# Performance work log

Measured on AMD Instinct MI355X. Metric: run time of the kernel, lower is better.

## Reference

```python
import jax, jax.numpy as jnp
import numpy as np

N_NODES = 100000
N_EDGES = 600000
FEAT_DIM = 128


def setup_inputs() -> dict:
    key = jax.random.key(0)
    k_x, k_e, k_w1, k_b1, k_w2, k_b2 = jax.random.split(key, 6)
    x = jax.random.normal(k_x, (N_NODES, FEAT_DIM), dtype=jnp.float32)
    edge_index = jax.random.randint(k_e, (2, N_EDGES), 0, N_NODES, dtype=jnp.int64)
    # nn.Linear default init: U(-1/sqrt(fan_in), 1/sqrt(fan_in))
    lim1 = 1.0 / np.sqrt(2 * FEAT_DIM)
    lim2 = 1.0 / np.sqrt(FEAT_DIM)
    W1 = jax.random.uniform(k_w1, (2 * FEAT_DIM, FEAT_DIM), minval=-lim1, maxval=lim1, dtype=jnp.float32)
    b1 = jax.random.uniform(k_b1, (FEAT_DIM,), minval=-lim1, maxval=lim1, dtype=jnp.float32)
    W2 = jax.random.uniform(k_w2, (FEAT_DIM, 1), minval=-lim2, maxval=lim2, dtype=jnp.float32)
    b2 = jax.random.uniform(k_b2, (1,), minval=-lim2, maxval=lim2, dtype=jnp.float32)
    return {"x": x, "edge_index": edge_index, "W1": W1, "b1": b1, "W2": W2, "b2": b2}


def reference(x, edge_index, W1, b1, W2, b2):
    row, col = edge_index[0], edge_index[1]
    # gather endpoint features and concat -> [E, 2*feat_dim]
    edge_feat = jnp.concatenate([x[row], x[col]], axis=1)
    h = jax.nn.relu(edge_feat @ W1 + b1)  # [E, feat_dim]
    return jax.nn.sigmoid(h @ W2 + b2)    # [E, 1]
```

## Files before the change

kernel.cpp:

```cpp
#include <hip/hip_runtime.h>
#include <stdint.h>

#define N_NODES 100000
#define N_EDGES 600000
#define FEAT 128
#define BLK_M 128

typedef __attribute__((ext_vector_type(8))) short short8;
typedef __attribute__((ext_vector_type(4))) short sv4;
typedef __attribute__((ext_vector_type(4))) float floatx4;

__device__ __forceinline__ short f2bf(float f) {
    unsigned u = __builtin_bit_cast(unsigned, f);
    u = (u + 0x7FFFu + ((u >> 16) & 1u)) >> 16;
    return (short)u;
}
__device__ __forceinline__ float bf2f(short s) {
    unsigned u = ((unsigned)(unsigned short)s) << 16;
    return __builtin_bit_cast(float, u);
}

__global__ __launch_bounds__(512, 4) void node_gemm_kernel(
    const float* __restrict__ x, const float* __restrict__ w1,
    const float* __restrict__ b1, short* __restrict__ y)
{
    __shared__ short lds_b[16 * 256 * 8];

    const int tid  = threadIdx.x;
    const int lane = tid & 63;
    const int wave = tid >> 6;
    const int nl   = lane & 15;
    const int q    = lane >> 4;
    const int m0   = blockIdx.x * BLK_M + wave * 16;

    const int node = m0 + nl;
    const int nsrc = (node < N_NODES) ? node : 0;
    floatx4 xv[8];
#pragma unroll
    for (int s = 0; s < 4; ++s) {
        const float* p = x + (size_t)nsrc * FEAT + s * 32 + q * 8;
        xv[2 * s]     = *(const floatx4*)(p);
        xv[2 * s + 1] = *(const floatx4*)(p + 4);
    }

#pragma unroll
    for (int it = 0; it < 8; ++it) {
        int t = it * 512 + tid;
        int n = t & 255, c = t >> 8;
        const float* src = (n < 128) ? (w1 + (c * 8) * 128 + n)
                                     : (w1 + (128 + c * 8) * 128 + (n - 128));
        short8 v;
#pragma unroll
        for (int j = 0; j < 8; ++j) v[j] = f2bf(src[j * 128]);
        *(short8*)(lds_b + t * 8) = v;
    }

    __syncthreads();

    short8 a[4];
#pragma unroll
    for (int s = 0; s < 4; ++s) {
        short8 av;
#pragma unroll
        for (int j = 0; j < 8; ++j) av[j] = f2bf(xv[2 * s + (j >> 2)][j & 3]);
        a[s] = av;
    }

    floatx4 acc[16];
#pragma unroll
    for (int nt = 0; nt < 16; ++nt) acc[nt] = (floatx4)(0.0f);

#pragma unroll
    for (int s = 0; s < 4; ++s) {
        const int crow = (s * 4 + q) << 8;
#pragma unroll
        for (int nt = 0; nt < 16; ++nt) {
            short8 wf = *(const short8*)(lds_b + ((crow + nt * 16 + nl) << 3));
            acc[nt] = __builtin_amdgcn_mfma_f32_16x16x32_bf16(wf, a[s], acc[nt], 0, 0, 0);
        }
    }

    if (node < N_NODES) {
        short* yr = y + (size_t)node * 256 + q * 4;
#pragma unroll
        for (int nt = 0; nt < 8; ++nt) {
            floatx4 bb = *(const floatx4*)(b1 + nt * 16 + q * 4);
            sv4 o;
            o[0] = f2bf(acc[nt][0] + bb[0]); o[1] = f2bf(acc[nt][1] + bb[1]);
            o[2] = f2bf(acc[nt][2] + bb[2]); o[3] = f2bf(acc[nt][3] + bb[3]);
            *(sv4*)(yr + nt * 16) = o;
        }
#pragma unroll
        for (int nt = 8; nt < 16; ++nt) {
            sv4 o;
            o[0] = f2bf(acc[nt][0]); o[1] = f2bf(acc[nt][1]);
            o[2] = f2bf(acc[nt][2]); o[3] = f2bf(acc[nt][3]);
            *(sv4*)(yr + nt * 16) = o;
        }
    }
}

__global__ __launch_bounds__(256) void edge_kernel(
    const short* __restrict__ y, const int* __restrict__ eidx,
    const float* __restrict__ w2, const float* __restrict__ b2,
    float* __restrict__ out)
{
    const int l = threadIdx.x & 15;

    float w2r[8];
#pragma unroll
    for (int j = 0; j < 8; ++j) w2r[j] = w2[l * 8 + j];
    const float bias2 = b2[0];

    const int slot   = blockIdx.x * 16 + (threadIdx.x >> 4);
    const int nslots = gridDim.x * 16;

    for (int eb = slot * 4; eb < N_EDGES; eb += nslots * 4) {
        int4 rr = *(const int4*)(eidx + eb);
        int4 cc = *(const int4*)(eidx + N_EDGES + eb);

        short8 u0 = *(const short8*)(y + (size_t)rr.x * 256 + l * 8);
        short8 u1 = *(const short8*)(y + (size_t)rr.y * 256 + l * 8);
        short8 u2 = *(const short8*)(y + (size_t)rr.z * 256 + l * 8);
        short8 u3 = *(const short8*)(y + (size_t)rr.w * 256 + l * 8);
        short8 v0 = *(const short8*)(y + (size_t)cc.x * 256 + 128 + l * 8);
        short8 v1 = *(const short8*)(y + (size_t)cc.y * 256 + 128 + l * 8);
        short8 v2 = *(const short8*)(y + (size_t)cc.z * 256 + 128 + l * 8);
        short8 v3 = *(const short8*)(y + (size_t)cc.w * 256 + 128 + l * 8);

        float p0 = 0.0f, p1 = 0.0f, p2 = 0.0f, p3 = 0.0f;
#pragma unroll
        for (int j = 0; j < 8; ++j) {
            p0 = fmaf(fmaxf(bf2f(u0[j]) + bf2f(v0[j]), 0.0f), w2r[j], p0);
            p1 = fmaf(fmaxf(bf2f(u1[j]) + bf2f(v1[j]), 0.0f), w2r[j], p1);
            p2 = fmaf(fmaxf(bf2f(u2[j]) + bf2f(v2[j]), 0.0f), w2r[j], p2);
            p3 = fmaf(fmaxf(bf2f(u3[j]) + bf2f(v3[j]), 0.0f), w2r[j], p3);
        }
#pragma unroll
        for (int d = 1; d < 16; d <<= 1) {
            p0 += __shfl_xor(p0, d);
            p1 += __shfl_xor(p1, d);
            p2 += __shfl_xor(p2, d);
            p3 += __shfl_xor(p3, d);
        }

        if (l == 0) {
            floatx4 o;
            o[0] = 1.0f / (1.0f + __expf(-(p0 + bias2)));
            o[1] = 1.0f / (1.0f + __expf(-(p1 + bias2)));
            o[2] = 1.0f / (1.0f + __expf(-(p2 + bias2)));
            o[3] = 1.0f / (1.0f + __expf(-(p3 + bias2)));
            *(floatx4*)(out + eb) = o;
        }
    }
}

extern "C" void kernel_launch(void* const* d_in, const int* in_sizes, int n_in,
                              void* d_out, int out_size, void* d_ws, size_t ws_size,
                              hipStream_t stream) {
    const float* x  = (const float*)d_in[0];
    const int*   ei = (const int*)d_in[1];
    const float* W1 = (const float*)d_in[2];
    const float* b1 = (const float*)d_in[3];
    const float* W2 = (const float*)d_in[4];
    const float* b2 = (const float*)d_in[5];
    float* out = (float*)d_out;

    short* ybf = (short*)d_ws;

    int mblocks = (N_NODES + BLK_M - 1) / BLK_M;
    node_gemm_kernel<<<mblocks, 512, 0, stream>>>(x, W1, b1, ybf);

    edge_kernel<<<2048, 256, 0, stream>>>(ybf, ei, W2, b2, out);
}
```

Before: 160.6 us.

## Fuse node GEMM and edge MLP into a single per-edge MFMA kernel

Replaces the two-kernel scheme with one persistent kernel. The old scheme precomputed per-node halves of the first layer into a bf16 table, then gathered and combined them per edge. The new kernel gathers fp32 node features for each edge endpoint, runs the full 256x128 first layer on the matrix cores per 16-edge tile, and applies ReLU, the second layer and the sigmoid in registers. This removes the intermediate table write/read and the second launch. In exchange it recomputes the GEMM for every edge rather than every node, and gathers fp32 rows instead of bf16 halves, which raises both FLOPs and gather traffic.

```diff
diff --git a/kernel.cpp b/kernel.cpp
--- a/kernel.cpp
+++ b/kernel.cpp
@@ -4,10 +4,10 @@
 #define N_NODES 100000
 #define N_EDGES 600000
 #define FEAT 128
-#define BLK_M 128
+#define GRID_F 1024
+#define NWTASK 37500
 
 typedef __attribute__((ext_vector_type(8))) short short8;
-typedef __attribute__((ext_vector_type(4))) short sv4;
 typedef __attribute__((ext_vector_type(4))) float floatx4;
 
 __device__ __forceinline__ short f2bf(float f) {
@@ -15,14 +15,12 @@
     u = (u + 0x7FFFu + ((u >> 16) & 1u)) >> 16;
     return (short)u;
 }
-__device__ __forceinline__ float bf2f(short s) {
-    unsigned u = ((unsigned)(unsigned short)s) << 16;
-    return __builtin_bit_cast(float, u);
-}
 
-__global__ __launch_bounds__(512, 4) void node_gemm_kernel(
-    const float* __restrict__ x, const float* __restrict__ w1,
-    const float* __restrict__ b1, short* __restrict__ y)
+__global__ __launch_bounds__(512, 2) void fused_edge_kernel(
+    const float* __restrict__ x, const int* __restrict__ eidx,
+    const float* __restrict__ w1, const float* __restrict__ b1,
+    const float* __restrict__ w2, const float* __restrict__ b2,
+    float* __restrict__ out)
 {
     __shared__ short lds_b[16 * 256 * 8];
 
@@ -31,17 +29,6 @@
     const int wave = tid >> 6;
     const int nl   = lane & 15;
     const int q    = lane >> 4;
-    const int m0   = blockIdx.x * BLK_M + wave * 16;
-
-    const int node = m0 + nl;
-    const int nsrc = (node < N_NODES) ? node : 0;
-    floatx4 xv[8];
-#pragma unroll
-    for (int s = 0; s < 4; ++s) {
-        const float* p = x + (size_t)nsrc * FEAT + s * 32 + q * 8;
-        xv[2 * s]     = *(const floatx4*)(p);
-        xv[2 * s + 1] = *(const floatx4*)(p + 4);
-    }
 
 #pragma unroll
     for (int it = 0; it < 8; ++it) {
@@ -55,102 +42,91 @@
         *(short8*)(lds_b + t * 8) = v;
     }
 
+    float w2v[8], b1v[8];
+#pragma unroll
+    for (int nt = 0; nt < 8; ++nt) {
+        w2v[nt] = w2[nt * 16 + nl];
+        b1v[nt] = b1[nt * 16 + nl];
+    }
+    const float bias2 = b2[0];
+
     __syncthreads();
 
-    short8 a[4];
+    const int w0     = blockIdx.x * 8 + wave;
+    const int wstep  = GRID_F * 8;
+
+    for (int t = w0; t < NWTASK; t += wstep) {
+        const int e0 = t * 16;
+        const int r = eidx[e0 + nl];
+        const int c = eidx[N_EDGES + e0 + nl];
+        const float* pr = x + (size_t)r * FEAT;
+        const float* pc = x + (size_t)c * FEAT;
+
+        floatx4 xr[8], xc[8];
 #pragma unroll
-    for (int s = 0; s < 4; ++s) {
-        short8 av;
+        for (int s = 0; s < 4; ++s) {
+            xr[2 * s]     = *(const floatx4*)(pr + s * 32 + q * 8);
+            xr[2 * s + 1] = *(const floatx4*)(pr + s * 32 + q * 8 + 4);
+            xc[2 * s]     = *(const floatx4*)(pc + s * 32 + q * 8);
+            xc[2 * s + 1] = *(const floatx4*)(pc + s * 32 + q * 8 + 4);
+        }
+        short8 a1[4], a2[4];
 #pragma unroll
-        for (int j = 0; j < 8; ++j) av[j] = f2bf(xv[2 * s + (j >> 2)][j & 3]);
-        a[s] = av;
-    }
+        for (int s = 0; s < 4; ++s) {
+            short8 v1, v2;
+#pragma unroll
+            for (int j = 0; j < 8; ++j) {
+                v1[j] = f2bf(xr[2 * s + (j >> 2)][j & 3]);
+                v2[j] = f2bf(xc[2 * s + (j >> 2)][j & 3]);
+            }
+            a1[s] = v1; a2[s] = v2;
+        }
 
-    floatx4 acc[16];
+        floatx4 acc[8];
 #pragma unroll
-    for (int nt = 0; nt < 16; ++nt) acc[nt] = (floatx4)(0.0f);
+        for (int nt = 0; nt < 8; ++nt) acc[nt] = (floatx4)(0.0f);
 
 #pragma unroll
-    for (int s = 0; s < 4; ++s) {
-        const int crow = (s * 4 + q) << 8;
+        for (int s = 0; s < 4; ++s) {
+            const int crow = (s * 4 + q) << 8;
 #pragma unroll
-        for (int nt = 0; nt < 16; ++nt) {
-            short8 wf = *(const short8*)(lds_b + ((crow + nt * 16 + nl) << 3));
-            acc[nt] = __builtin_amdgcn_mfma_f32_16x16x32_bf16(wf, a[s], acc[nt], 0, 0, 0);
+            for (int nt = 0; nt < 8; ++nt) {
+                short8 bf = *(const short8*)(lds_b + ((crow + nt * 16 + nl) << 3));
+                acc[nt] = __builtin_amdgcn_mfma_f32_16x16x32_bf16(a1[s], bf, acc[nt], 0, 0, 0);
+            }
         }
-    }
+#pragma unroll
+        for (int s = 0; s < 4; ++s) {
+            const int crow = (s * 4 + q) << 8;
+#pragma unroll
+            for (int nt = 0; nt < 8; ++nt) {
+                short8 bf = *(const short8*)(lds_b + ((crow + 128 + nt * 16 + nl) << 3));
+                acc[nt] = __builtin_amdgcn_mfma_f32_16x16x32_bf16(a2[s], bf, acc[nt], 0, 0, 0);
+            }
+        }
 
-    if (node < N_NODES) {
-        short* yr = y + (size_t)node * 256 + q * 4;
+        float p[4] = {0.0f, 0.0f, 0.0f, 0.0f};
 #pragma unroll
         for (int nt = 0; nt < 8; ++nt) {
-            floatx4 bb = *(const floatx4*)(b1 + nt * 16 + q * 4);
-            sv4 o;
-            o[0] = f2bf(acc[nt][0] + bb[0]); o[1] = f2bf(acc[nt][1] + bb[1]);
-            o[2] = f2bf(acc[nt][2] + bb[2]); o[3] = f2bf(acc[nt][3] + bb[3]);
-            *(sv4*)(yr + nt * 16) = o;
-        }
 #pragma unroll
-        for (int nt = 8; nt < 16; ++nt) {
-            sv4 o;
-            o[0] = f2bf(acc[nt][0]); o[1] = f2bf(acc[nt][1]);
-            o[2] = f2bf(acc[nt][2]); o[3] = f2bf(acc[nt][3]);
-            *(sv4*)(yr + nt * 16) = o;
-        }
-    }
-}
-
-__global__ __launch_bounds__(256) void edge_kernel(
-    const short* __restrict__ y, const int* __restrict__ eidx,
-    const float* __restrict__ w2, const float* __restrict__ b2,
-    float* __restrict__ out)
-{
-    const int l = threadIdx.x & 15;
-
-    float w2r[8];
-#pragma unroll
-    for (int j = 0; j < 8; ++j) w2r[j] = w2[l * 8 + j];
-    const float bias2 = b2[0];
-
-    const int slot   = blockIdx.x * 16 + (threadIdx.x >> 4);
-    const int nslots = gridDim.x * 16;
-
-    for (int eb = slot * 4; eb < N_EDGES; eb += nslots * 4) {
-        int4 rr = *(const int4*)(eidx + eb);
-        int4 cc = *(const int4*)(eidx + N_EDGES + eb);
-
-        short8 u0 = *(const short8*)(y + (size_t)rr.x * 256 + l * 8);
-        short8 u1 = *(const short8*)(y + (size_t)rr.y * 256 + l * 8);
-        short8 u2 = *(const short8*)(y + (size_t)rr.z * 256 + l * 8);
-        short8 u3 = *(const short8*)(y + (size_t)rr.w * 256 + l * 8);
-        short8 v0 = *(const short8*)(y + (size_t)cc.x * 256 + 128 + l * 8);
-        short8 v1 = *(const short8*)(y + (size_t)cc.y * 256 + 128 + l * 8);
-        short8 v2 = *(const short8*)(y + (size_t)cc.z * 256 + 128 + l * 8);
-        short8 v3 = *(const short8*)(y + (size_t)cc.w * 256 + 128 + l * 8);
-
-        float p0 = 0.0f, p1 = 0.0f, p2 = 0.0f, p3 = 0.0f;
-#pragma unroll
-        for (int j = 0; j < 8; ++j) {
-            p0 = fmaf(fmaxf(bf2f(u0[j]) + bf2f(v0[j]), 0.0f), w2r[j], p0);
-            p1 = fmaf(fmaxf(bf2f(u1[j]) + bf2f(v1[j]), 0.0f), w2r[j], p1);
-            p2 = fmaf(fmaxf(bf2f(u2[j]) + bf2f(v2[j]), 0.0f), w2r[j], p2);
-            p3 = fmaf(fmaxf(bf2f(u3[j]) + bf2f(v3[j]), 0.0f), w2r[j], p3);
+            for (int r4 = 0; r4 < 4; ++r4) {
+                float h = acc[nt][r4] + b1v[nt];
+                p[r4] = fmaf(fmaxf(h, 0.0f), w2v[nt], p[r4]);
+            }
         }
 #pragma unroll
         for (int d = 1; d < 16; d <<= 1) {
-            p0 += __shfl_xor(p0, d);
-            p1 += __shfl_xor(p1, d);
-            p2 += __shfl_xor(p2, d);
-            p3 += __shfl_xor(p3, d);
+#pragma unroll
+            for (int r4 = 0; r4 < 4; ++r4) p[r4] += __shfl_xor(p[r4], d);
         }
 
-        if (l == 0) {
+        if (nl == 0) {
             floatx4 o;
-            o[0] = 1.0f / (1.0f + __expf(-(p0 + bias2)));
-            o[1] = 1.0f / (1.0f + __expf(-(p1 + bias2)));
-            o[2] = 1.0f / (1.0f + __expf(-(p2 + bias2)));
-            o[3] = 1.0f / (1.0f + __expf(-(p3 + bias2)));
-            *(floatx4*)(out + eb) = o;
+            o[0] = 1.0f / (1.0f + __expf(-(p[0] + bias2)));
+            o[1] = 1.0f / (1.0f + __expf(-(p[1] + bias2)));
+            o[2] = 1.0f / (1.0f + __expf(-(p[2] + bias2)));
+            o[3] = 1.0f / (1.0f + __expf(-(p[3] + bias2)));
+            *(floatx4*)(out + e0 + q * 4) = o;
         }
     }
 }
@@ -166,10 +142,5 @@
     const float* b2 = (const float*)d_in[5];
     float* out = (float*)d_out;
 
-    short* ybf = (short*)d_ws;
-
-    int mblocks = (N_NODES + BLK_M - 1) / BLK_M;
-    node_gemm_kernel<<<mblocks, 512, 0, stream>>>(x, W1, b1, ybf);
-
-    edge_kernel<<<2048, 256, 0, stream>>>(ybf, ei, W2, b2, out);
+    fused_edge_kernel<<<GRID_F, 512, 0, stream>>>(x, ei, W1, b1, W2, b2, out);
 }
```

After: 362.5 us. 126% more time.
